# Optimization experiments

Hardware: AMD Instinct MI355X
Metric: run time of the kernel (lower is better)

The kernel has to match this reference:

```python
import math
import jax, jax.numpy as jnp
import numpy as np

R = 15  # static Gaussian truncation radius (covers 3*sigma for resolutions up to ~12)
SIG_PER_FWHM = 1.0 / math.sqrt(8.0 * math.log(2.0))  # sigma = fwhm / sqrt(8 ln 2)


def _blur_resample_axis0(img, sigma, res):
    """Gaussian blur (dct2/symmetric boundary) + down/up resize along axis 0.

    img: [H, W]; sigma, res: scalars. anchor='f' resize convention:
      down (factor=1/res): low coord j samples input at j*res
      up   (factor=res, shape=H): out coord i samples low grid at i/res
    Low-res grid has n_low = max(floor(H/res), 1) valid rows; positions are
    clamped to the valid range (edge boundary).
    """
    H, W = img.shape
    dt = img.dtype
    # --- separable 1D Gaussian blur along axis 0 ---
    off = jnp.arange(-R, R + 1, dtype=dt)
    sig = jnp.maximum(sigma, jnp.asarray(1e-6, dt))
    w = jnp.exp(-0.5 * (off / sig) ** 2)
    w = w / w.sum()
    pad = jnp.pad(img, ((R, R), (0, 0)), mode='symmetric')  # dct2 boundary
    s = w[0] * pad[0:H]
    for k in range(1, 2 * R + 1):
        s = s + w[k] * pad[k:k + H]
    # --- downsample (factor = 1/res, anchor 'f') ---
    Hf = jnp.asarray(H, dt)
    n_low = jnp.maximum(jnp.floor(Hf / res), 1.0).astype(jnp.int32)
    pos = jnp.clip(jnp.arange(H, dtype=dt) * res, 0.0, Hf - 1.0)
    lo = jnp.floor(pos)
    fr = (pos - lo)[:, None]
    lo_i = lo.astype(jnp.int32)
    hi_i = jnp.minimum(lo_i + 1, H - 1)
    low = s[lo_i] * (1.0 - fr) + s[hi_i] * fr  # [H, W], rows >= n_low unused
    # --- upsample back to H (factor = res, anchor 'f') ---
    pos2 = jnp.clip(jnp.arange(H, dtype=dt) / res, 0.0, n_low.astype(dt) - 1.0)
    lo2 = jnp.floor(pos2)
    fr2 = (pos2 - lo2)[:, None]
    lo2_i = jnp.minimum(lo2.astype(jnp.int32), n_low - 1)
    hi2_i = jnp.minimum(lo2_i + 1, n_low - 1)
    return low[lo2_i] * (1.0 - fr2) + low[hi2_i] * fr2


def _process_one(img, res, ax, gp):
    fwhm = res * gp
    sigma = fwhm * SIG_PER_FWHM
    out0 = _blur_resample_axis0(img, sigma, res)          # degrade axis 0 (H)
    out1 = _blur_resample_axis0(img.T, sigma, res).T      # degrade axis 1 (W)
    return jnp.where(ax == 0, out0, out1)


def setup_inputs() -> dict:
    key = jax.random.key(0)
    k_x, k_res, k_ax, k_gap = jax.random.split(key, 4)
    B, C, H, W = 16, 4, 512, 512
    x = jax.random.normal(k_x, (B, C, H, W), dtype=jnp.float32)
    # lognormal with mean 3, sd 3 -> underlying normal params
    m, sdev = 3.0, 3.0
    var_log = math.log(1.0 + (sdev / m) ** 2)
    mu = math.log(m) - 0.5 * var_log
    z = jax.random.normal(k_res, (B, C), dtype=jnp.float32)
    resolution = jnp.clip(jnp.exp(mu + math.sqrt(var_log) * z), 1.0, None)
    axis = jax.random.randint(k_ax, (B, C), 0, 2, dtype=jnp.int32)
    gap = jax.random.uniform(k_gap, (B, C), dtype=jnp.float32)
    return {"x": x, "resolution": resolution, "axis": axis, "gap": gap}


def reference(x, resolution, axis, gap):
    B, C, H, W = x.shape
    flat = x.reshape(B * C, H, W)
    out = jax.vmap(_process_one)(flat, resolution.reshape(-1), axis.reshape(-1), gap.reshape(-1))
    return out.reshape(B, C, H, W)
```

## Files before the change

### kernel.cpp

```cpp
#include <hip/hip_runtime.h>
#include <math.h>


#define RR 15
#define TAPS 31
#define SIG_PER_FWHM 0.42466090014400953f

__global__ __launch_bounds__(256) void lowres2d_kernel(
    const float* __restrict__ x,
    const float* __restrict__ resolution,
    const int*   __restrict__ axis,
    const float* __restrict__ gap,
    float* __restrict__ out)
{
    const int tid = threadIdx.x;
    const int n   = blockIdx.y;
    const int bx  = blockIdx.x;

    const float res = resolution[n];
    const int   ax  = axis[n];
    const float gp  = gap[n];

    if (ax == 0 && bx >= 64) return;

    const float sig = fmaxf(res * gp * SIG_PER_FWHM, 1e-6f);
    int n_low = (int)floorf(512.0f / res);
    if (n_low < 1) n_low = 1;
    if (n_low > 512) n_low = 512;
    const float nlm1f = (float)(n_low - 1);

    int kr = (int)(sig * 5.2565f) + 1;
    if (kr > RR) kr = RR;
    const int k0 = RR - kr, k1 = RR + 1 + kr;
    const int la_lo = kr, la_hi = 510 - kr;

    __shared__ float2 wd[32];
    __shared__ float smem[4608];
    float (*s_img)[520]  = (float (*)[520])smem;
    float (*s_low)[516]  = (float (*)[516])(smem + 4 * 520);
    float (*s_lowB)[512] = (float (*)[512])smem;

    if (tid < 32) {
        const int k = tid;
        float r = 0.0f;
        if (k < TAPS) {
            float d = (float)(k - RR) / sig;
            r = expf(-0.5f * d * d);
        }
        float tot = r;
        tot += __shfl_xor(tot, 1, 32);
        tot += __shfl_xor(tot, 2, 32);
        tot += __shfl_xor(tot, 4, 32);
        tot += __shfl_xor(tot, 8, 32);
        tot += __shfl_xor(tot, 16, 32);
        float rm1 = __shfl_up(r, 1, 32);
        if (k == 0) rm1 = 0.0f;
        const float inv = 1.0f / tot;
        wd[k] = make_float2(r * inv, (rm1 - r) * inv);
    }
    __syncthreads();

    const size_t base = (size_t)n * (512 * 512);
    const float* img = x + base;
    float* o = out + base;

    if (ax == 0) {
        const int i0 = bx * 8;
        const int c  = tid;
        const float2* img2 = (const float2*)img;
        float2* out2 = (float2*)o;

        float pA = fminf((float)i0 / res, nlm1f);
        int jlo = (int)floorf(pA);
        float pB = fminf((float)(i0 + 7) / res, nlm1f);
        int jhi = (int)floorf(pB) + 1;
        if (jhi > n_low - 1) jhi = n_low - 1;
        if (jhi < jlo) jhi = jlo;

        for (int j = jlo; j <= jhi; ++j) {
            float pos = fminf((float)j * res, 511.0f);
            float lof = floorf(pos);
            float fr  = pos - lof;
            int   la  = (int)lof;
            float2 acc = make_float2(0.0f, 0.0f);
            if (la >= la_lo && la <= la_hi) {
                #pragma unroll 4
                for (int k = k0; k <= k1; ++k) {
                    int t = la - RR + k;
                    float2 w = wd[k];
                    float cw = fmaf(fr, w.y, w.x);
                    float2 v = img2[(size_t)(t * 256 + c)];
                    acc.x = fmaf(cw, v.x, acc.x);
                    acc.y = fmaf(cw, v.y, acc.y);
                }
            } else {
                for (int k = k0; k <= k1; ++k) {
                    int t = la - RR + k;
                    t = (t < 0)   ? (-1 - t)   : t;
                    t = (t > 511) ? (1023 - t) : t;
                    float2 w = wd[k];
                    float cw = fmaf(fr, w.y, w.x);
                    float2 v = img2[(size_t)(t * 256 + c)];
                    acc.x = fmaf(cw, v.x, acc.x);
                    acc.y = fmaf(cw, v.y, acc.y);
                }
            }
            ((float2*)&s_lowB[j - jlo][0])[c] = acc;
        }
        __syncthreads();

        #pragma unroll
        for (int ii = 0; ii < 8; ++ii) {
            int i = i0 + ii;
            float pos2 = fminf((float)i / res, nlm1f);
            float l2f  = floorf(pos2);
            float fr2  = pos2 - l2f;
            int lo2 = (int)l2f;
            int hi2 = (lo2 + 1 <= jhi) ? (lo2 + 1) : jhi;
            float2 A = ((float2*)&s_lowB[lo2 - jlo][0])[c];
            float2 B = ((float2*)&s_lowB[hi2 - jlo][0])[c];
            float omf2 = 1.0f - fr2;
            out2[(size_t)(i * 256 + c)] =
                make_float2(A.x * omf2 + B.x * fr2,
                            A.y * omf2 + B.y * fr2);
        }
    } else {
        const int h0 = bx * 4;

        const float4* img4 = (const float4*)(img + (size_t)h0 * 512);
        #pragma unroll
        for (int p = 0; p < 2; ++p) {
            int m = p * 256 + tid;
            int r = m >> 7, c4 = m & 127;
            ((float4*)&s_img[r][0])[c4] = img4[r * 128 + c4];
        }
        __syncthreads();

        {
            const int r = __builtin_amdgcn_readfirstlane(tid >> 6);
            for (int j = (tid & 63); j < n_low; j += 64) {
                float pos = fminf((float)j * res, 511.0f);
                float lof = floorf(pos);
                float fr  = pos - lof;
                int   la  = (int)lof;
                float acc = 0.0f;
                if (la >= la_lo && la <= la_hi) {
                    #pragma unroll 4
                    for (int k = k0; k <= k1; ++k) {
                        int t = la - RR + k;
                        float2 w = wd[k];
                        float cw = fmaf(fr, w.y, w.x);
                        acc = fmaf(cw, s_img[r][t], acc);
                    }
                } else {
                    for (int k = k0; k <= k1; ++k) {
                        int t = la - RR + k;
                        t = (t < 0)   ? (-1 - t)   : t;
                        t = (t > 511) ? (1023 - t) : t;
                        float2 w = wd[k];
                        float cw = fmaf(fr, w.y, w.x);
                        acc = fmaf(cw, s_img[r][t], acc);
                    }
                }
                s_low[r][j] = acc;
            }
        }
        __syncthreads();

        float4* out4 = (float4*)(o + (size_t)h0 * 512);
        #pragma unroll
        for (int p = 0; p < 2; ++p) {
            int m = p * 256 + tid;
            int r = m >> 7, c4 = m & 127;
            float vals[4];
            #pragma unroll
            for (int q = 0; q < 4; ++q) {
                int i = c4 * 4 + q;
                float pos2 = fminf((float)i / res, nlm1f);
                float l2f  = floorf(pos2);
                float fr2  = pos2 - l2f;
                int lo2 = (int)l2f;
                if (lo2 > n_low - 1) lo2 = n_low - 1;
                int hi2 = (lo2 + 1 < n_low) ? (lo2 + 1) : (n_low - 1);
                vals[q] = s_low[r][lo2] * (1.0f - fr2) + s_low[r][hi2] * fr2;
            }
            float4 ov;
            ov.x = vals[0]; ov.y = vals[1]; ov.z = vals[2]; ov.w = vals[3];
            out4[r * 128 + c4] = ov;
        }
    }
}

extern "C" void kernel_launch(void* const* d_in, const int* in_sizes, int n_in,
                              void* d_out, int out_size, void* d_ws, size_t ws_size,
                              hipStream_t stream) {
    const float* x          = (const float*)d_in[0];
    const float* resolution = (const float*)d_in[1];
    const int*   axis       = (const int*)d_in[2];
    const float* gap        = (const float*)d_in[3];
    float* out = (float*)d_out;

    const int n_img = in_sizes[1];

    dim3 grid(128, n_img);
    lowres2d_kernel<<<grid, 256, 0, stream>>>(x, resolution, axis, gap, out);
}
```

Baseline: 131.8 us.

## Widen axis-0 path to float4 with two row groups, precompute upsample positions

The axis-0 branch now has each thread load float4 instead of float2. The block splits into two 128-thread groups that compute alternate low-res rows, and the row's base index is made wave-uniform with readfirstlane. The axis-1 branch precomputes the upsample positions once into shared memory, which removes per-element divides. The grid is also transposed so image index is blockIdx.x, which changes block scheduling order and locality across images. The risk is idle threads when the block has an odd number of low rows, and slightly more shared memory per block.

Result: slower. 142.5 us (+8.1%).

```diff
diff --git a/kernel.cpp b/kernel.cpp
--- a/kernel.cpp
+++ b/kernel.cpp
@@ -14,8 +14,8 @@
     float* __restrict__ out)
 {
     const int tid = threadIdx.x;
-    const int n   = blockIdx.y;
-    const int bx  = blockIdx.x;
+    const int n   = blockIdx.x;
+    const int bx  = blockIdx.y;
 
     const float res = resolution[n];
     const int   ax  = axis[n];
@@ -35,9 +35,10 @@
     const int la_lo = kr, la_hi = 510 - kr;
 
     __shared__ float2 wd[32];
-    __shared__ float smem[4608];
+    __shared__ float smem[4656];
     float (*s_img)[520]  = (float (*)[520])smem;
-    float (*s_low)[516]  = (float (*)[516])(smem + 4 * 520);
+    float (*s_low)[516]  = (float (*)[516])(smem + 2080);
+    float *s_pos2        = smem + 4144;
     float (*s_lowB)[512] = (float (*)[512])smem;
 
     if (tid < 32) {
@@ -66,9 +67,10 @@
 
     if (ax == 0) {
         const int i0 = bx * 8;
-        const int c  = tid;
-        const float2* img2 = (const float2*)img;
-        float2* out2 = (float2*)o;
+        const int g  = tid >> 7;
+        const int lt = tid & 127;
+        const float4* img4 = (const float4*)img;
+        float4* out4 = (float4*)o;
 
         float pA = fminf((float)i0 / res, nlm1f);
         int jlo = (int)floorf(pA);
@@ -76,22 +78,27 @@
         int jhi = (int)floorf(pB) + 1;
         if (jhi > n_low - 1) jhi = n_low - 1;
         if (jhi < jlo) jhi = jlo;
-
-        for (int j = jlo; j <= jhi; ++j) {
+        const int nrows = jhi - jlo + 1;
+
+        for (int p = 0; p < nrows; p += 2) {
+            int rowoff = p + g;
+            int j = jlo + ((rowoff < nrows) ? rowoff : (nrows - 1));
             float pos = fminf((float)j * res, 511.0f);
             float lof = floorf(pos);
             float fr  = pos - lof;
-            int   la  = (int)lof;
-            float2 acc = make_float2(0.0f, 0.0f);
+            int   la  = __builtin_amdgcn_readfirstlane((int)lof);
+            float4 acc = make_float4(0.0f, 0.0f, 0.0f, 0.0f);
             if (la >= la_lo && la <= la_hi) {
                 #pragma unroll 4
                 for (int k = k0; k <= k1; ++k) {
                     int t = la - RR + k;
                     float2 w = wd[k];
                     float cw = fmaf(fr, w.y, w.x);
-                    float2 v = img2[(size_t)(t * 256 + c)];
+                    float4 v = img4[(size_t)(t * 128 + lt)];
                     acc.x = fmaf(cw, v.x, acc.x);
                     acc.y = fmaf(cw, v.y, acc.y);
+                    acc.z = fmaf(cw, v.z, acc.z);
+                    acc.w = fmaf(cw, v.w, acc.w);
                 }
             } else {
                 for (int k = k0; k <= k1; ++k) {
@@ -100,29 +107,36 @@
                     t = (t > 511) ? (1023 - t) : t;
                     float2 w = wd[k];
                     float cw = fmaf(fr, w.y, w.x);
-                    float2 v = img2[(size_t)(t * 256 + c)];
+                    float4 v = img4[(size_t)(t * 128 + lt)];
                     acc.x = fmaf(cw, v.x, acc.x);
                     acc.y = fmaf(cw, v.y, acc.y);
+                    acc.z = fmaf(cw, v.z, acc.z);
+                    acc.w = fmaf(cw, v.w, acc.w);
                 }
             }
-            ((float2*)&s_lowB[j - jlo][0])[c] = acc;
+            if (rowoff < nrows) {
+                ((float4*)&s_lowB[rowoff][0])[lt] = acc;
+            }
         }
         __syncthreads();
 
         #pragma unroll
-        for (int ii = 0; ii < 8; ++ii) {
-            int i = i0 + ii;
+        for (int p = 0; p < 4; ++p) {
+            int i = i0 + p * 2 + g;
             float pos2 = fminf((float)i / res, nlm1f);
             float l2f  = floorf(pos2);
             float fr2  = pos2 - l2f;
             int lo2 = (int)l2f;
             int hi2 = (lo2 + 1 <= jhi) ? (lo2 + 1) : jhi;
-            float2 A = ((float2*)&s_lowB[lo2 - jlo][0])[c];
-            float2 B = ((float2*)&s_lowB[hi2 - jlo][0])[c];
+            float4 A = ((float4*)&s_lowB[lo2 - jlo][0])[lt];
+            float4 B = ((float4*)&s_lowB[hi2 - jlo][0])[lt];
             float omf2 = 1.0f - fr2;
-            out2[(size_t)(i * 256 + c)] =
-                make_float2(A.x * omf2 + B.x * fr2,
-                            A.y * omf2 + B.y * fr2);
+            float4 ov;
+            ov.x = A.x * omf2 + B.x * fr2;
+            ov.y = A.y * omf2 + B.y * fr2;
+            ov.z = A.z * omf2 + B.z * fr2;
+            ov.w = A.w * omf2 + B.w * fr2;
+            out4[(size_t)(i * 128 + lt)] = ov;
         }
     } else {
         const int h0 = bx * 4;
@@ -133,6 +147,11 @@
             int m = p * 256 + tid;
             int r = m >> 7, c4 = m & 127;
             ((float4*)&s_img[r][0])[c4] = img4[r * 128 + c4];
+        }
+        #pragma unroll
+        for (int p = 0; p < 2; ++p) {
+            int m = p * 256 + tid;
+            s_pos2[m] = fminf((float)m / res, nlm1f);
         }
         __syncthreads();
 
@@ -172,15 +191,15 @@
         for (int p = 0; p < 2; ++p) {
             int m = p * 256 + tid;
             int r = m >> 7, c4 = m & 127;
+            float4 p2 = ((const float4*)s_pos2)[c4];
+            float p2a[4] = {p2.x, p2.y, p2.z, p2.w};
             float vals[4];
             #pragma unroll
             for (int q = 0; q < 4; ++q) {
-                int i = c4 * 4 + q;
-                float pos2 = fminf((float)i / res, nlm1f);
+                float pos2 = p2a[q];
                 float l2f  = floorf(pos2);
                 float fr2  = pos2 - l2f;
                 int lo2 = (int)l2f;
-                if (lo2 > n_low - 1) lo2 = n_low - 1;
                 int hi2 = (lo2 + 1 < n_low) ? (lo2 + 1) : (n_low - 1);
                 vals[q] = s_low[r][lo2] * (1.0f - fr2) + s_low[r][hi2] * fr2;
             }
@@ -202,6 +221,6 @@
 
     const int n_img = in_sizes[1];
 
-    dim3 grid(128, n_img);
+    dim3 grid(n_img, 128);
     lowres2d_kernel<<<grid, 256, 0, stream>>>(x, resolution, axis, gap, out);
 }
```
